# Kernel optimization log

Measured on AMD Instinct MI355X. Metric: run time of the kernel, lower is better.

## Reference

```python
import jax, jax.numpy as jnp
import numpy as np

N, E, F_IN, F_EXP, H, C = 8192, 65536, 3247, 7993, 3, 512
HC = H * C
NEG_SLOPE = 0.2


def setup_inputs() -> dict:
    key = jax.random.key(0)
    ks = jax.random.split(key, 40)
    s = 0.02
    rnd = lambda k, *sh: (jax.random.normal(k, sh, jnp.float32) * s)
    d = {}
    d['x'] = jax.random.normal(ks[0], (N, F_IN), jnp.float32)
    d['edge_index'] = jax.random.randint(ks[1], (2, E), 0, N, jnp.int32)
    d['exp'] = jax.random.normal(ks[2], (N, F_EXP), jnp.float32)
    # GATv2 layer 1 (in=3247)
    d['w1l'] = rnd(ks[3], F_IN, HC); d['b1l'] = rnd(ks[4], HC)
    d['w1r'] = rnd(ks[5], F_IN, HC); d['b1r'] = rnd(ks[6], HC)
    d['a1'] = rnd(ks[7], H, C);      d['o1'] = rnd(ks[8], HC)
    # GATv2 layer 2 (in=1536)
    d['w2l'] = rnd(ks[9], HC, HC);  d['b2l'] = rnd(ks[10], HC)
    d['w2r'] = rnd(ks[11], HC, HC); d['b2r'] = rnd(ks[12], HC)
    d['a2'] = rnd(ks[13], H, C);     d['o2'] = rnd(ks[14], HC)
    # GATv2 layer 3 (in=1536)
    d['w3l'] = rnd(ks[15], HC, HC); d['b3l'] = rnd(ks[16], HC)
    d['w3r'] = rnd(ks[17], HC, HC); d['b3r'] = rnd(ks[18], HC)
    d['a3'] = rnd(ks[19], H, C);     d['o3'] = rnd(ks[20], HC)
    # encoder: 7993 -> 4000 -> 1500 -> 512
    d['e1w'] = rnd(ks[21], F_EXP, 4000); d['e1b'] = rnd(ks[22], 4000)
    d['e2w'] = rnd(ks[23], 4000, 1500);  d['e2b'] = rnd(ks[24], 1500)
    d['e3w'] = rnd(ks[25], 1500, 512);   d['e3b'] = rnd(ks[26], 512)
    # head: 2048 -> 1024 -> 512 -> 1
    d['l1w'] = rnd(ks[27], HC + 512, 1024); d['l1b'] = rnd(ks[28], 1024)
    d['l2w'] = rnd(ks[29], 1024, 512);      d['l2b'] = rnd(ks[30], 512)
    d['l3w'] = rnd(ks[31], 512, 1);         d['l3b'] = rnd(ks[32], 1)
    return d


def gatv2(h, src, dst, wl, bl, wr, br, att, out_bias):
    # PyG GATv2Conv: e_ij = a^T LeakyReLU(W_l h_j + W_r h_i), softmax over j per target i,
    # out_i = sum_j alpha_ij * (W_l h_j), concat heads, + bias.
    xl = (h @ wl + bl).reshape(N, H, C)
    xr = (h @ wr + br).reshape(N, H, C)
    e = jax.nn.leaky_relu(xl[src] + xr[dst], NEG_SLOPE)      # [E', H, C]
    logit = jnp.einsum('ehc,hc->eh', e, att)                  # [E', H]
    m = jax.ops.segment_max(logit, dst, num_segments=N)       # [N, H]
    p = jnp.exp(logit - m[dst])
    z = jax.ops.segment_sum(p, dst, num_segments=N)
    alpha = p / z[dst]                                        # segment softmax
    out = jax.ops.segment_sum(alpha[:, :, None] * xl[src], dst, num_segments=N)
    return out.reshape(N, HC) + out_bias


def reference(x, edge_index, exp,
              w1l, b1l, w1r, b1r, a1, o1,
              w2l, b2l, w2r, b2r, a2, o2,
              w3l, b3l, w3r, b3r, a3, o3,
              e1w, e1b, e2w, e2b, e3w, e3b,
              l1w, l1b, l2w, l2b, l3w, l3b):
    loops = jnp.arange(N, dtype=edge_index.dtype)
    src = jnp.concatenate([edge_index[0], loops])  # add_self_loops=True (PyG default)
    dst = jnp.concatenate([edge_index[1], loops])
    h = jax.nn.relu(gatv2(x, src, dst, w1l, b1l, w1r, b1r, a1, o1))
    h = jax.nn.relu(gatv2(h, src, dst, w2l, b2l, w2r, b2r, a2, o2))
    h = jax.nn.relu(gatv2(h, src, dst, w3l, b3l, w3r, b3r, a3, o3))
    cell = jax.nn.relu(exp @ e1w + e1b)
    cell = jax.nn.relu(cell @ e2w + e2b)
    cell = cell @ e3w + e3b
    z = jnp.concatenate([h, cell], axis=1)  # [N, 2048]
    z = jax.nn.relu(z @ l1w + l1b)
    z = jax.nn.relu(z @ l2w + l2b)
    return z @ l3w + l3b  # [N, 1]
```

## Files before the change

kernel.cpp:

```cpp
#include <hip/hip_runtime.h>
#include <stdint.h>

#define NN 8192
#define NE 65536
#define ET (NE + NN)
#define F_IN   3247
#define F_IN_P 3264
#define F_EXP   7993
#define F_EXP_P 8000

typedef __attribute__((ext_vector_type(8))) short bf16x8;
typedef __attribute__((ext_vector_type(4))) float f32x4;

typedef const __attribute__((address_space(1))) void gvoid_t;
typedef __attribute__((address_space(3))) void lvoid_t;

__device__ __forceinline__ float bf2f(uint16_t u) {
  union { uint32_t i; float f; } v; v.i = ((uint32_t)u) << 16; return v.f;
}
__device__ __forceinline__ uint16_t f2bf(float f) {
  union { float f; uint32_t i; } v; v.f = f;
  uint32_t r = v.i + 0x7fffu + ((v.i >> 16) & 1u);
  return (uint16_t)(r >> 16);
}

__device__ __forceinline__ void gld_lds16(const void* g, void* l) {
  __builtin_amdgcn_global_load_lds((gvoid_t*)g, (lvoid_t*)l, 16, 0, 0);
}

#define SBAR() __builtin_amdgcn_sched_barrier(0)
#define BARRIER() do { SBAR(); __builtin_amdgcn_s_barrier(); SBAR(); } while (0)
#define VMCNT(n) asm volatile("s_waitcnt vmcnt(" #n ")" ::: "memory")
#define MFMA16(a, b, c) __builtin_amdgcn_mfma_f32_16x16x32_bf16(a, b, c, 0, 0, 0)

__device__ __forceinline__ void stage4(const char* src, char* dst, size_t Kb) {
#pragma unroll
  for (int j = 0; j < 4; ++j)
    gld_lds16(src + (size_t)(j * 64) * Kb, dst + j * 8192);
}

#define KTILE(T, BUF)                                                          \
  do {                                                                         \
    const char* aB_  = smem + (BUF) + arow;                                    \
    const char* bB_  = smem + 65536 + (BUF) + brow_o;                          \
    const char* aBn_ = smem + ((BUF) ^ 32768) + arow;                          \
    const bool nls = ((T) + 2 < nk);                                           \
    const bool nlr = ((T) + 1 < nk);                                           \
                        \
    if (nlr) { VMCNT(8); } else { VMCNT(0); }                                  \
    _Pragma("unroll")                                                          \
    for (int n = 0; n < 2; ++n) {                                              \
      b01[n * 2]     = *(const bf16x8*)(bB_ + n * 2048 + sw0);                 \
      b01[n * 2 + 1] = *(const bf16x8*)(bB_ + n * 2048 + sw1);                 \
    }                                                                          \
    _Pragma("unroll")                                                          \
    for (int n = 0; n < 2; ++n) {                                              \
      b23[n * 2]     = *(const bf16x8*)(bB_ + (n + 2) * 2048 + sw0);           \
      b23[n * 2 + 1] = *(const bf16x8*)(bB_ + (n + 2) * 2048 + sw1);           \
    }                                                                          \
    SBAR();                                                                    \
    __builtin_amdgcn_s_setprio(1);                                             \
    _Pragma("unroll")                                                          \
    for (int m = 0; m < 4; ++m)                                                \
      _Pragma("unroll")                                                        \
      for (int n = 0; n < 2; ++n) {                                            \
        acc[m][n] = MFMA16(a03[m * 2],     b01[n * 2],     acc[m][n]);         \
        acc[m][n] = MFMA16(a03[m * 2 + 1], b01[n * 2 + 1], acc[m][n]);         \
      }                                                                        \
    __builtin_amdgcn_s_setprio(0);                                             \
    BARRIER();                                                                 \
                                        \
    _Pragma("unroll")                                                          \
    for (int m = 0; m < 4; ++m) {                                              \
      a47[m * 2]     = *(const bf16x8*)(aB_ + (m + 4) * 2048 + sw0);           \
      a47[m * 2 + 1] = *(const bf16x8*)(aB_ + (m + 4) * 2048 + sw1);           \
    }                                                                          \
    SBAR();                                                                    \
    __builtin_amdgcn_s_setprio(1);                                             \
    _Pragma("unroll")                                                          \
    for (int m = 0; m < 4; ++m)                                                \
      _Pragma("unroll")                                                        \
      for (int n = 0; n < 2; ++n) {                                            \
        acc[m][n + 2] = MFMA16(a03[m * 2],     b23[n * 2],     acc[m][n + 2]); \
        acc[m][n + 2] = MFMA16(a03[m * 2 + 1], b23[n * 2 + 1], acc[m][n + 2]); \
      }                                                                        \
    __builtin_amdgcn_s_setprio(0);                                             \
    BARRIER();                                                                 \
                       \
    if (nls) stage4(pA + (size_t)((T) + 2) * 128, sA + (BUF), Kb);             \
    _Pragma("unroll")                                                          \
    for (int n = 0; n < 2; ++n) {                                              \
      b01[n * 2]     = *(const bf16x8*)(bB_ + n * 2048 + sw0);                 \
      b01[n * 2 + 1] = *(const bf16x8*)(bB_ + n * 2048 + sw1);                 \
    }                                                                          \
    SBAR();                                                                    \
    __builtin_amdgcn_s_setprio(1);                                             \
    _Pragma("unroll")                                                          \
    for (int m = 0; m < 4; ++m)                                                \
      _Pragma("unroll")                                                        \
      for (int n = 0; n < 2; ++n) {                                            \
        acc[m + 4][n + 2] = MFMA16(a47[m * 2],     b23[n * 2],     acc[m + 4][n + 2]); \
        acc[m + 4][n + 2] = MFMA16(a47[m * 2 + 1], b23[n * 2 + 1], acc[m + 4][n + 2]); \
      }                                                                        \
    __builtin_amdgcn_s_setprio(0);                                             \
    BARRIER();                                                                 \
       \
    if (nls)      { VMCNT(8); }                                                \
    else if (nlr) { VMCNT(4); }                                                \
    if (nlr) {                                                                 \
      _Pragma("unroll")                                                        \
      for (int m = 0; m < 4; ++m) {                                            \
        a03[m * 2]     = *(const bf16x8*)(aBn_ + m * 2048 + sw0);              \
        a03[m * 2 + 1] = *(const bf16x8*)(aBn_ + m * 2048 + sw1);              \
      }                                                                        \
    }                                                                          \
    if (nls) stage4(pB + (size_t)((T) + 2) * 128, sB + (BUF), Kb);             \
    SBAR();                                                                    \
    __builtin_amdgcn_s_setprio(1);                                             \
    _Pragma("unroll")                                                          \
    for (int m = 0; m < 4; ++m)                                                \
      _Pragma("unroll")                                                        \
      for (int n = 0; n < 2; ++n) {                                            \
        acc[m + 4][n] = MFMA16(a47[m * 2],     b01[n * 2],     acc[m + 4][n]); \
        acc[m + 4][n] = MFMA16(a47[m * 2 + 1], b01[n * 2 + 1], acc[m + 4][n]); \
      }                                                                        \
    __builtin_amdgcn_s_setprio(0);                                             \
    BARRIER();                                                                 \
  } while (0)

__global__ __launch_bounds__(512, 2)
void gemm256(const uint16_t* __restrict__ A, const uint16_t* __restrict__ Bt,
             const float* __restrict__ bias, int biasN, int relu,
             uint16_t* __restrict__ C, int Kp, int ldc, int nbn)
{
  extern __shared__ char smem[];
  const int tid = threadIdx.x;
  const int w = tid >> 6, lane = tid & 63;
  const int wr = w >> 2, wc = w & 3;
  const int fr = lane & 15, g = lane >> 4;

  const int nwg = (int)gridDim.x;
  const int id = (int)blockIdx.x;
  const int q = nwg >> 3, r = nwg & 7;
  const int xcd = id & 7, idx = id >> 3;
  const int wg = (xcd < r ? xcd * (q + 1) : r * (q + 1) + (xcd - r) * q) + idx;
  const int brow = (wg / nbn) * 256, bcol = (wg % nbn) * 256;

  const size_t Kb = (size_t)Kp * 2;

  const int srow = tid >> 3;
  const int sswz = ((tid & 7) ^ (srow & 7)) * 16;
  const char* pA = (const char*)A + (size_t)(brow + srow) * Kb + sswz;
  const char* pB = (const char*)Bt + (size_t)(bcol + srow) * Kb + sswz;
  char* sA = smem + w * 1024;
  char* sB = smem + 65536 + w * 1024;

  const int sw0 = (g ^ (fr & 7)) * 16;
  const int sw1 = ((g + 4) ^ (fr & 7)) * 16;
  const int arow = (wr * 128 + fr) * 128;
  const int brow_o = (wc * 64 + fr) * 128;

  f32x4 acc[8][4];
#pragma unroll
  for (int m = 0; m < 8; ++m)
#pragma unroll
    for (int n = 0; n < 4; ++n) acc[m][n] = (f32x4){0.f, 0.f, 0.f, 0.f};
  bf16x8 a03[8], a47[8], b01[4], b23[4];

  stage4(pA, sA, Kb);
  stage4(pB, sB, Kb);
  stage4(pA + 128, sA + 32768, Kb);
  stage4(pB + 128, sB + 32768, Kb);
  VMCNT(8);
  BARRIER();
  {
    const char* aB = smem + arow;
#pragma unroll
    for (int m = 0; m < 4; ++m) {
      a03[m * 2]     = *(const bf16x8*)(aB + m * 2048 + sw0);
      a03[m * 2 + 1] = *(const bf16x8*)(aB + m * 2048 + sw1);
    }
  }
  SBAR();

  const int nk = Kp >> 6;
  for (int t = 0; t < nk; t += 2) {
    KTILE(t, 0);
    if (t + 1 < nk) KTILE(t + 1, 32768);
  }

#pragma unroll
  for (int m = 0; m < 8; ++m) {
    const int row = brow + wr * 128 + m * 16 + g * 4;
#pragma unroll
    for (int n = 0; n < 4; ++n) {
      const int col = bcol + wc * 64 + n * 16 + fr;
      const float bv = (col < biasN) ? bias[col] : 0.f;
#pragma unroll
      for (int j = 0; j < 4; ++j) {
        float v = acc[m][n][j] + bv;
        if (relu) v = fmaxf(v, 0.f);
        C[(size_t)(row + j) * ldc + col] = f2bf(v);
      }
    }
  }
}

__global__ __launch_bounds__(256)
void gemm_bt(const uint16_t* __restrict__ A, const uint16_t* __restrict__ Bt,
             const float* __restrict__ bias, int biasN, int relu,
             uint16_t* __restrict__ C, int Kp, int ldc)
{
  __shared__ uint16_t As[128 * 32];
  __shared__ uint16_t Bs[128 * 32];
  const int tid  = threadIdx.x;
  const int wave = tid >> 6, lane = tid & 63;
  const int brow = blockIdx.x * 128, bcol = blockIdx.y * 128;
  const int wr = wave >> 1, wc = wave & 1;
  const int fr = lane & 15, g = lane >> 4;

  f32x4 acc[4][4];
#pragma unroll
  for (int m = 0; m < 4; ++m)
#pragma unroll
    for (int n = 0; n < 4; ++n) acc[m][n] = (f32x4){0.f, 0.f, 0.f, 0.f};

  const int rA = tid >> 2;
  const int kc = (tid & 3) * 8;
  const uint16_t* aptr = A  + (size_t)(brow + rA) * Kp + kc;
  const uint16_t* bptr = Bt + (size_t)(bcol + rA) * Kp + kc;
  char* ldsA = (char*)As + wave * 1024;
  char* ldsB = (char*)Bs + wave * 1024;
  const size_t rowskip = (size_t)64 * Kp;

  const int nk = Kp >> 5;
  for (int kt = 0; kt < nk; ++kt) {
    __syncthreads();
    gld_lds16(aptr,           ldsA);
    gld_lds16(aptr + rowskip, ldsA + 4096);
    gld_lds16(bptr,           ldsB);
    gld_lds16(bptr + rowskip, ldsB + 4096);
    aptr += 32; bptr += 32;
    __syncthreads();

    bf16x8 af[4], bfr[4];
#pragma unroll
    for (int m = 0; m < 4; ++m)
      af[m] = *(const bf16x8*)&As[(wr * 64 + m * 16 + fr) * 32 + g * 8];
#pragma unroll
    for (int n = 0; n < 4; ++n)
      bfr[n] = *(const bf16x8*)&Bs[(wc * 64 + n * 16 + fr) * 32 + g * 8];
#pragma unroll
    for (int m = 0; m < 4; ++m)
#pragma unroll
      for (int n = 0; n < 4; ++n)
        acc[m][n] = MFMA16(af[m], bfr[n], acc[m][n]);
  }

#pragma unroll
  for (int m = 0; m < 4; ++m) {
    const int row = brow + wr * 64 + m * 16 + g * 4;
#pragma unroll
    for (int n = 0; n < 4; ++n) {
      const int col = bcol + wc * 64 + n * 16 + fr;
      const float bv = (col < biasN) ? bias[col] : 0.f;
#pragma unroll
      for (int j = 0; j < 4; ++j) {
        float v = acc[m][n][j] + bv;
        if (relu) v = fmaxf(v, 0.f);
        C[(size_t)(row + j) * ldc + col] = f2bf(v);
      }
    }
  }
}

__global__ __launch_bounds__(256)
void cvt_pad(const float* __restrict__ in, uint16_t* __restrict__ out, int cols, int colsPad)
{
  const int r = blockIdx.y;
  const int c = (blockIdx.x * 256 + threadIdx.x) * 2;
  if (c >= colsPad) return;
  const float* ip = in + (size_t)r * cols;
  const float v0 = (c < cols)     ? ip[c]     : 0.f;
  const float v1 = (c + 1 < cols) ? ip[c + 1] : 0.f;
  const uint32_t pk = (uint32_t)f2bf(v0) | ((uint32_t)f2bf(v1) << 16);
  *(uint32_t*)(out + (size_t)r * colsPad + c) = pk;
}

__global__ __launch_bounds__(256)
void transpose_w(const float* __restrict__ W, uint16_t* __restrict__ Wt,
                 int K, int N, int Kp, int Np)
{
  __shared__ float t[32][33];
  const int tx = threadIdx.x, ty = threadIdx.y;
  const int k0 = blockIdx.x * 32, n0 = blockIdx.y * 32;
#pragma unroll
  for (int j = 0; j < 4; ++j) {
    const int k = k0 + ty + j * 8, n = n0 + tx;
    t[ty + j * 8][tx] = (k < K && n < N) ? W[(size_t)k * N + n] : 0.f;
  }
  __syncthreads();
#pragma unroll
  for (int j = 0; j < 4; ++j) {
    const int n = n0 + ty + j * 8, k = k0 + tx;
    Wt[(size_t)n * Kp + k] = f2bf(t[tx][ty + j * 8]);
  }
}

__global__ void concat_bias(const float* __restrict__ bl, const float* __restrict__ br,
                            float* __restrict__ out)
{
  const int i = blockIdx.x * 256 + threadIdx.x;
  if (i < 1536) out[i] = bl[i];
  else if (i < 3072) out[i] = br[i - 1536];
}

__global__ void count_deg(const int* __restrict__ ei, int* __restrict__ counts)
{
  const int e = blockIdx.x * 256 + threadIdx.x;
  if (e >= ET) return;
  const int d = (e < NE) ? ei[NE + e] : (e - NE);
  atomicAdd(&counts[d], 1);
}

__global__ __launch_bounds__(1024)
void scan_deg(const int* __restrict__ counts, int* __restrict__ row_start, int* __restrict__ cursor)
{
  __shared__ int part[1024];
  const int tid = threadIdx.x;
  int loc[8], pre[8], s = 0;
#pragma unroll
  for (int j = 0; j < 8; ++j) { loc[j] = counts[tid * 8 + j]; pre[j] = s; s += loc[j]; }
  part[tid] = s;
  __syncthreads();
  for (int o = 1; o < 1024; o <<= 1) {
    const int v = part[tid];
    const int a = (tid >= o) ? part[tid - o] : 0;
    __syncthreads();
    part[tid] = v + a;
    __syncthreads();
  }
  const int excl = part[tid] - s;
#pragma unroll
  for (int j = 0; j < 8; ++j) {
    const int v = excl + pre[j];
    row_start[tid * 8 + j] = v;
    cursor[tid * 8 + j]    = v;
  }
  if (tid == 1023) row_start[8192] = excl + s;
}

__global__ void scatter_e(const int* __restrict__ ei, int* __restrict__ cursor,
                          int* __restrict__ csr_src, int* __restrict__ csr_dst)
{
  const int e = blockIdx.x * 256 + threadIdx.x;
  if (e >= ET) return;
  const int sx = (e < NE) ? ei[e]      : (e - NE);
  const int d  = (e < NE) ? ei[NE + e] : (e - NE);
  const int pos = atomicAdd(&cursor[d], 1);
  csr_src[pos] = sx;
  csr_dst[pos] = d;
}

__global__ __launch_bounds__(256)
void gat_logits_n(const uint16_t* __restrict__ xlr, int ld,
                  const int* __restrict__ csr_src, const int* __restrict__ row_start,
                  const float* __restrict__ att, float* __restrict__ logit)
{
  const int node = (blockIdx.x << 2) + (threadIdx.x >> 6);
  const int lane = threadIdx.x & 63;

  float av[3][8];
#pragma unroll
  for (int h = 0; h < 3; ++h) {
    const float4 a0 = *(const float4*)(att + h * 512 + lane * 8);
    const float4 a1 = *(const float4*)(att + h * 512 + lane * 8 + 4);
    av[h][0] = a0.x; av[h][1] = a0.y; av[h][2] = a0.z; av[h][3] = a0.w;
    av[h][4] = a1.x; av[h][5] = a1.y; av[h][6] = a1.z; av[h][7] = a1.w;
  }

  const bf16x8* pr = (const bf16x8*)(xlr + (size_t)node * ld + 1536);
  float xr[3][8];
#pragma unroll
  for (int h = 0; h < 3; ++h) {
    const bf16x8 v = pr[h * 64 + lane];
#pragma unroll
    for (int j = 0; j < 8; ++j) xr[h][j] = bf2f((uint16_t)v[j]);
  }

  const int s0 = row_start[node], s1 = row_start[node + 1];
  for (int s = s0; s < s1; ++s) {
    const bf16x8* pl = (const bf16x8*)(xlr + (size_t)csr_src[s] * ld);
    float hacc[3];
#pragma unroll
    for (int h = 0; h < 3; ++h) {
      const bf16x8 vl = pl[h * 64 + lane];
      float sacc = 0.f;
#pragma unroll
      for (int j = 0; j < 8; ++j) {
        float v = bf2f((uint16_t)vl[j]) + xr[h][j];
        v = v > 0.f ? v : 0.2f * v;
        sacc += v * av[h][j];
      }
      hacc[h] = sacc;
    }
#pragma unroll
    for (int o = 32; o; o >>= 1) {
      hacc[0] += __shfl_xor(hacc[0], o);
      hacc[1] += __shfl_xor(hacc[1], o);
      hacc[2] += __shfl_xor(hacc[2], o);
    }
    if (lane == 0) {
      float* op = logit + (size_t)s * 3;
      op[0] = hacc[0]; op[1] = hacc[1]; op[2] = hacc[2];
    }
  }
}

__global__ __launch_bounds__(256)
void gat_aggregate(const float* __restrict__ logit, const int* __restrict__ csr_src,
                   const int* __restrict__ row_start, const uint16_t* __restrict__ xl, int ldx,
                   const float* __restrict__ ob, uint16_t* __restrict__ out, int ldc)
{
  const int i = blockIdx.x;
  const int tid = threadIdx.x;
  const int s0 = row_start[i], s1 = row_start[i + 1];

  float m0 = -1e30f, m1 = -1e30f, m2 = -1e30f, z0 = 0.f, z1 = 0.f, z2 = 0.f;
  for (int s = s0; s < s1; ++s) {
    const float* lp = logit + (size_t)s * 3;
    float l0 = lp[0], l1 = lp[1], l2 = lp[2];
    float n0 = fmaxf(m0, l0); z0 = z0 * __expf(m0 - n0) + __expf(l0 - n0); m0 = n0;
    float n1 = fmaxf(m1, l1); z1 = z1 * __expf(m1 - n1) + __expf(l1 - n1); m1 = n1;
    float n2 = fmaxf(m2, l2); z2 = z2 * __expf(m2 - n2) + __expf(l2 - n2); m2 = n2;
  }
  const float r0 = 1.f / z0, r1 = 1.f / z1, r2 = 1.f / z2;

  float accl[3], acch[3];
#pragma unroll
  for (int h = 0; h < 3; ++h) { accl[h] = 0.f; acch[h] = 0.f; }
  for (int s = s0; s < s1; ++s) {
    const float* lp = logit + (size_t)s * 3;
    float wv[3];
    wv[0] = __expf(lp[0] - m0) * r0;
    wv[1] = __expf(lp[1] - m1) * r1;
    wv[2] = __expf(lp[2] - m2) * r2;
    const uint32_t* px = (const uint32_t*)(xl + (size_t)csr_src[s] * ldx);
#pragma unroll
    for (int h = 0; h < 3; ++h) {
      const uint32_t u = px[h * 256 + tid];
      accl[h] += wv[h] * bf2f((uint16_t)u);
      acch[h] += wv[h] * bf2f((uint16_t)(u >> 16));
    }
  }
#pragma unroll
  for (int h = 0; h < 3; ++h) {
    const int c = h * 512 + 2 * tid;
    float v0 = fmaxf(accl[h] + ob[c], 0.f);
    float v1 = fmaxf(acch[h] + ob[c + 1], 0.f);
    const uint32_t pk = (uint32_t)f2bf(v0) | ((uint32_t)f2bf(v1) << 16);
    *(uint32_t*)(out + (size_t)i * ldc + c) = pk;
  }
}

__global__ __launch_bounds__(256)
void final_dot(const uint16_t* __restrict__ z2, const float* __restrict__ w,
               const float* __restrict__ b, float* __restrict__ out)
{
  const int row  = blockIdx.x * 4 + (threadIdx.x >> 6);
  const int lane = threadIdx.x & 63;
  const uint16_t* p = z2 + (size_t)row * 512;
  float s = 0.f;
#pragma unroll
  for (int j = 0; j < 8; ++j) { const int c = lane + j * 64; s += bf2f(p[c]) * w[c]; }
#pragma unroll
  for (int o = 32; o; o >>= 1) s += __shfl_xor(s, o);
  if (lane == 0) out[row] = s + b[0];
}

extern "C" void kernel_launch(void* const* d_in, const int* in_sizes, int n_in,
                              void* d_out, int out_size, void* d_ws, size_t ws_size,
                              hipStream_t stream)
{
  (void)in_sizes; (void)n_in; (void)out_size; (void)ws_size;

  const float* x    = (const float*)d_in[0];
  const int*   ei   = (const int*)  d_in[1];
  const float* expm = (const float*)d_in[2];
  const float* w1l = (const float*)d_in[3];  const float* b1l = (const float*)d_in[4];
  const float* w1r = (const float*)d_in[5];  const float* b1r = (const float*)d_in[6];
  const float* a1  = (const float*)d_in[7];  const float* o1  = (const float*)d_in[8];
  const float* w2l = (const float*)d_in[9];  const float* b2l = (const float*)d_in[10];
  const float* w2r = (const float*)d_in[11]; const float* b2r = (const float*)d_in[12];
  const float* a2  = (const float*)d_in[13]; const float* o2  = (const float*)d_in[14];
  const float* w3l = (const float*)d_in[15]; const float* b3l = (const float*)d_in[16];
  const float* w3r = (const float*)d_in[17]; const float* b3r = (const float*)d_in[18];
  const float* a3  = (const float*)d_in[19]; const float* o3  = (const float*)d_in[20];
  const float* e1w = (const float*)d_in[21]; const float* e1b = (const float*)d_in[22];
  const float* e2w = (const float*)d_in[23]; const float* e2b = (const float*)d_in[24];
  const float* e3w = (const float*)d_in[25]; const float* e3b = (const float*)d_in[26];
  const float* l1w = (const float*)d_in[27]; const float* l1b = (const float*)d_in[28];
  const float* l2w = (const float*)d_in[29]; const float* l2b = (const float*)d_in[30];
  const float* l3w = (const float*)d_in[31]; const float* l3b = (const float*)d_in[32];
  float* out = (float*)d_out;

  hipFuncSetAttribute((const void*)gemm256, hipFuncAttributeMaxDynamicSharedMemorySize, 131072);

  char* ws = (char*)d_ws;
  size_t off = 0;
  auto take = [&](size_t b) { char* p = ws + off; off += (b + 255) & ~(size_t)255; return p; };

  int*      counts    = (int*)take((size_t)NN * 4);
  int*      row_start = (int*)take((size_t)(NN + 1) * 4);
  int*      cursor    = (int*)take((size_t)NN * 4);
  int*      csr_src   = (int*)take((size_t)ET * 4);
  int*      csr_dst   = (int*)take((size_t)ET * 4);
  float*    logits    = (float*)take((size_t)ET * 3 * 4);
  float*    bc1       = (float*)take(3072 * 4);
  float*    bc2       = (float*)take(3072 * 4);
  float*    bc3       = (float*)take(3072 * 4);
  uint16_t* zbuf      = (uint16_t*)take((size_t)NN * 2048 * 2);
  char*     regA      = take((size_t)NN * F_EXP_P * 2);
  char*     regW      = take((size_t)4096 * F_EXP_P * 2);
  char*     regC      = take((size_t)NN * 4096 * 2 + (size_t)NN * 1536 * 2);

  uint16_t* xbf   = (uint16_t*)regA;
  uint16_t* expbf = (uint16_t*)regA;
  uint16_t* wT    = (uint16_t*)regW;
  uint16_t* xlr   = (uint16_t*)regC;
  uint16_t* hbuf  = (uint16_t*)(regC + (size_t)NN * 3072 * 2);
  uint16_t* cell1 = (uint16_t*)regC;
  uint16_t* cell2 = (uint16_t*)(regC + (size_t)NN * 4096 * 2);
  uint16_t* zz1   = (uint16_t*)regC;
  uint16_t* zz2   = (uint16_t*)(regC + (size_t)NN * 1024 * 2);

  hipMemsetAsync(counts, 0, (size_t)NN * 4, stream);
  count_deg<<<(ET + 255) / 256, 256, 0, stream>>>(ei, counts);
  scan_deg<<<1, 1024, 0, stream>>>(counts, row_start, cursor);
  scatter_e<<<(ET + 255) / 256, 256, 0, stream>>>(ei, cursor, csr_src, csr_dst);
  concat_bias<<<12, 256, 0, stream>>>(b1l, b1r, bc1);
  concat_bias<<<12, 256, 0, stream>>>(b2l, b2r, bc2);
  concat_bias<<<12, 256, 0, stream>>>(b3l, b3r, bc3);

  cvt_pad<<<dim3((F_IN_P / 2 + 255) / 256, NN), 256, 0, stream>>>(x, xbf, F_IN, F_IN_P);
  transpose_w<<<dim3(F_IN_P / 32, 1536 / 32), dim3(32, 8), 0, stream>>>(w1l, wT, F_IN, 1536, F_IN_P, 1536);
  transpose_w<<<dim3(F_IN_P / 32, 1536 / 32), dim3(32, 8), 0, stream>>>(w1r, wT + (size_t)1536 * F_IN_P, F_IN, 1536, F_IN_P, 1536);
  gemm256<<<32 * 12, 512, 131072, stream>>>(xbf, wT, bc1, 3072, 0, xlr, F_IN_P, 3072, 12);
  gat_logits_n<<<NN / 4, 256, 0, stream>>>(xlr, 3072, csr_src, row_start, a1, logits);
  gat_aggregate<<<NN, 256, 0, stream>>>(logits, csr_src, row_start, xlr, 3072, o1, hbuf, 1536);

  transpose_w<<<dim3(48, 48), dim3(32, 8), 0, stream>>>(w2l, wT, 1536, 1536, 1536, 1536);
  transpose_w<<<dim3(48, 48), dim3(32, 8), 0, stream>>>(w2r, wT + (size_t)1536 * 1536, 1536, 1536, 1536, 1536);
  gemm256<<<32 * 12, 512, 131072, stream>>>(hbuf, wT, bc2, 3072, 0, xlr, 1536, 3072, 12);
  gat_logits_n<<<NN / 4, 256, 0, stream>>>(xlr, 3072, csr_src, row_start, a2, logits);
  gat_aggregate<<<NN, 256, 0, stream>>>(logits, csr_src, row_start, xlr, 3072, o2, hbuf, 1536);

  transpose_w<<<dim3(48, 48), dim3(32, 8), 0, stream>>>(w3l, wT, 1536, 1536, 1536, 1536);
  transpose_w<<<dim3(48, 48), dim3(32, 8), 0, stream>>>(w3r, wT + (size_t)1536 * 1536, 1536, 1536, 1536, 1536);
  gemm256<<<32 * 12, 512, 131072, stream>>>(hbuf, wT, bc3, 3072, 0, xlr, 1536, 3072, 12);
  gat_logits_n<<<NN / 4, 256, 0, stream>>>(xlr, 3072, csr_src, row_start, a3, logits);
  gat_aggregate<<<NN, 256, 0, stream>>>(logits, csr_src, row_start, xlr, 3072, o3, zbuf, 2048);

  cvt_pad<<<dim3((F_EXP_P / 2 + 255) / 256, NN), 256, 0, stream>>>(expm, expbf, F_EXP, F_EXP_P);
  transpose_w<<<dim3(F_EXP_P / 32, 4096 / 32), dim3(32, 8), 0, stream>>>(e1w, wT, F_EXP, 4000, F_EXP_P, 4096);
  gemm256<<<32 * 16, 512, 131072, stream>>>(expbf, wT, e1b, 4000, 1, cell1, F_EXP_P, 4096, 16);
  transpose_w<<<dim3(4096 / 32, 1536 / 32), dim3(32, 8), 0, stream>>>(e2w, wT, 4000, 1500, 4096, 1536);
  gemm256<<<32 * 6, 512, 131072, stream>>>(cell1, wT, e2b, 1500, 1, cell2, 4096, 1536, 6);
  transpose_w<<<dim3(1536 / 32, 512 / 32), dim3(32, 8), 0, stream>>>(e3w, wT, 1500, 512, 1536, 512);
  gemm_bt<<<dim3(64, 4), 256, 0, stream>>>(cell2, wT, e3b, 512, 0, zbuf + 1536, 1536, 2048);

  transpose_w<<<dim3(2048 / 32, 1024 / 32), dim3(32, 8), 0, stream>>>(l1w, wT, 2048, 1024, 2048, 1024);
  gemm256<<<32 * 4, 512, 131072, stream>>>(zbuf, wT, l1b, 1024, 1, zz1, 2048, 1024, 4);
  transpose_w<<<dim3(1024 / 32, 512 / 32), dim3(32, 8), 0, stream>>>(l2w, wT, 1024, 512, 1024, 512);
  gemm_bt<<<dim3(64, 4), 256, 0, stream>>>(zz1, wT, l2b, 512, 1, zz2, 1024, 512);
  final_dot<<<NN / 4, 256, 0, stream>>>(zz2, l3w, l3b, out);
}
```

Baseline: 1.547 ms.

## Fuse GAT logits and softmax-aggregate into one online-softmax kernel

Merges the per-edge logit kernel and the aggregate kernel into a single wave-per-node kernel. It computes each edge's logit and folds it straight into an online softmax with accumulation over the same loaded source features. This removes the logits buffer round trip, a second gather of xl rows, and one launch per layer. Separately, it switches the head's first linear layer from gemm256 to the gemm_bt kernel with a different grid, which may suit the small 1024-column output better or worse.

```diff
diff --git a/kernel.cpp b/kernel.cpp
--- a/kernel.cpp
+++ b/kernel.cpp
@@ -363,42 +363,49 @@
 }
 
 __global__ __launch_bounds__(256)
-void gat_logits_n(const uint16_t* __restrict__ xlr, int ld,
-                  const int* __restrict__ csr_src, const int* __restrict__ row_start,
-                  const float* __restrict__ att, float* __restrict__ logit)
+void gat_fused(const uint16_t* __restrict__ xlr, int ld,
+               const int* __restrict__ csr_src, const int* __restrict__ row_start,
+               const float* __restrict__ att, const float* __restrict__ ob,
+               uint16_t* __restrict__ out, int ldc)
 {
   const int node = (blockIdx.x << 2) + (threadIdx.x >> 6);
   const int lane = threadIdx.x & 63;
 
-  float av[3][8];
+  float av[3][8], xr[3][8];
+  const bf16x8* pr = (const bf16x8*)(xlr + (size_t)node * ld + 1536);
 #pragma unroll
   for (int h = 0; h < 3; ++h) {
     const float4 a0 = *(const float4*)(att + h * 512 + lane * 8);
     const float4 a1 = *(const float4*)(att + h * 512 + lane * 8 + 4);
     av[h][0] = a0.x; av[h][1] = a0.y; av[h][2] = a0.z; av[h][3] = a0.w;
     av[h][4] = a1.x; av[h][5] = a1.y; av[h][6] = a1.z; av[h][7] = a1.w;
-  }
-
-  const bf16x8* pr = (const bf16x8*)(xlr + (size_t)node * ld + 1536);
-  float xr[3][8];
-#pragma unroll
-  for (int h = 0; h < 3; ++h) {
     const bf16x8 v = pr[h * 64 + lane];
 #pragma unroll
     for (int j = 0; j < 8; ++j) xr[h][j] = bf2f((uint16_t)v[j]);
   }
+
+  float m[3] = {-1e30f, -1e30f, -1e30f};
+  float z[3] = {0.f, 0.f, 0.f};
+  float acc[3][8];
+#pragma unroll
+  for (int h = 0; h < 3; ++h)
+#pragma unroll
+    for (int j = 0; j < 8; ++j) acc[h][j] = 0.f;
 
   const int s0 = row_start[node], s1 = row_start[node + 1];
   for (int s = s0; s < s1; ++s) {
     const bf16x8* pl = (const bf16x8*)(xlr + (size_t)csr_src[s] * ld);
+    bf16x8 vl[3];
+#pragma unroll
+    for (int h = 0; h < 3; ++h) vl[h] = pl[h * 64 + lane];
+
     float hacc[3];
 #pragma unroll
     for (int h = 0; h < 3; ++h) {
-      const bf16x8 vl = pl[h * 64 + lane];
       float sacc = 0.f;
 #pragma unroll
       for (int j = 0; j < 8; ++j) {
-        float v = bf2f((uint16_t)vl[j]) + xr[h][j];
+        float v = bf2f((uint16_t)vl[h][j]) + xr[h][j];
         v = v > 0.f ? v : 0.2f * v;
         sacc += v * av[h][j];
       }
@@ -410,56 +417,32 @@
       hacc[1] += __shfl_xor(hacc[1], o);
       hacc[2] += __shfl_xor(hacc[2], o);
     }
-    if (lane == 0) {
-      float* op = logit + (size_t)s * 3;
-      op[0] = hacc[0]; op[1] = hacc[1]; op[2] = hacc[2];
-    }
-  }
-}
-
-__global__ __launch_bounds__(256)
-void gat_aggregate(const float* __restrict__ logit, const int* __restrict__ csr_src,
-                   const int* __restrict__ row_start, const uint16_t* __restrict__ xl, int ldx,
-                   const float* __restrict__ ob, uint16_t* __restrict__ out, int ldc)
-{
-  const int i = blockIdx.x;
-  const int tid = threadIdx.x;
-  const int s0 = row_start[i], s1 = row_start[i + 1];
-
-  float m0 = -1e30f, m1 = -1e30f, m2 = -1e30f, z0 = 0.f, z1 = 0.f, z2 = 0.f;
-  for (int s = s0; s < s1; ++s) {
-    const float* lp = logit + (size_t)s * 3;
-    float l0 = lp[0], l1 = lp[1], l2 = lp[2];
-    float n0 = fmaxf(m0, l0); z0 = z0 * __expf(m0 - n0) + __expf(l0 - n0); m0 = n0;
-    float n1 = fmaxf(m1, l1); z1 = z1 * __expf(m1 - n1) + __expf(l1 - n1); m1 = n1;
-    float n2 = fmaxf(m2, l2); z2 = z2 * __expf(m2 - n2) + __expf(l2 - n2); m2 = n2;
-  }
-  const float r0 = 1.f / z0, r1 = 1.f / z1, r2 = 1.f / z2;
-
-  float accl[3], acch[3];
-#pragma unroll
-  for (int h = 0; h < 3; ++h) { accl[h] = 0.f; acch[h] = 0.f; }
-  for (int s = s0; s < s1; ++s) {
-    const float* lp = logit + (size_t)s * 3;
-    float wv[3];
-    wv[0] = __expf(lp[0] - m0) * r0;
-    wv[1] = __expf(lp[1] - m1) * r1;
-    wv[2] = __expf(lp[2] - m2) * r2;
-    const uint32_t* px = (const uint32_t*)(xl + (size_t)csr_src[s] * ldx);
 #pragma unroll
     for (int h = 0; h < 3; ++h) {
-      const uint32_t u = px[h * 256 + tid];
-      accl[h] += wv[h] * bf2f((uint16_t)u);
-      acch[h] += wv[h] * bf2f((uint16_t)(u >> 16));
-    }
-  }
+      const float nm = fmaxf(m[h], hacc[h]);
+      const float sc = __expf(m[h] - nm);
+      const float p  = __expf(hacc[h] - nm);
+      z[h] = z[h] * sc + p;
+#pragma unroll
+      for (int j = 0; j < 8; ++j)
+        acc[h][j] = acc[h][j] * sc + p * bf2f((uint16_t)vl[h][j]);
+      m[h] = nm;
+    }
+  }
+
 #pragma unroll
   for (int h = 0; h < 3; ++h) {
-    const int c = h * 512 + 2 * tid;
-    float v0 = fmaxf(accl[h] + ob[c], 0.f);
-    float v1 = fmaxf(acch[h] + ob[c + 1], 0.f);
-    const uint32_t pk = (uint32_t)f2bf(v0) | ((uint32_t)f2bf(v1) << 16);
-    *(uint32_t*)(out + (size_t)i * ldc + c) = pk;
+    const float rz = 1.f / z[h];
+    const float4 b0 = *(const float4*)(ob + h * 512 + lane * 8);
+    const float4 b1 = *(const float4*)(ob + h * 512 + lane * 8 + 4);
+    float bv[8] = {b0.x, b0.y, b0.z, b0.w, b1.x, b1.y, b1.z, b1.w};
+    bf16x8 pk;
+#pragma unroll
+    for (int j = 0; j < 8; ++j) {
+      const float v = fmaxf(acc[h][j] * rz + bv[j], 0.f);
+      pk[j] = (short)f2bf(v);
+    }
+    *(bf16x8*)(out + (size_t)node * ldc + h * 512 + lane * 8) = pk;
   }
 }
 
@@ -515,7 +498,6 @@
   int*      cursor    = (int*)take((size_t)NN * 4);
   int*      csr_src   = (int*)take((size_t)ET * 4);
   int*      csr_dst   = (int*)take((size_t)ET * 4);
-  float*    logits    = (float*)take((size_t)ET * 3 * 4);
   float*    bc1       = (float*)take(3072 * 4);
   float*    bc2       = (float*)take(3072 * 4);
   float*    bc3       = (float*)take(3072 * 4);
@@ -546,20 +528,17 @@
   transpose_w<<<dim3(F_IN_P / 32, 1536 / 32), dim3(32, 8), 0, stream>>>(w1l, wT, F_IN, 1536, F_IN_P, 1536);
   transpose_w<<<dim3(F_IN_P / 32, 1536 / 32), dim3(32, 8), 0, stream>>>(w1r, wT + (size_t)1536 * F_IN_P, F_IN, 1536, F_IN_P, 1536);
   gemm256<<<32 * 12, 512, 131072, stream>>>(xbf, wT, bc1, 3072, 0, xlr, F_IN_P, 3072, 12);
-  gat_logits_n<<<NN / 4, 256, 0, stream>>>(xlr, 3072, csr_src, row_start, a1, logits);
-  gat_aggregate<<<NN, 256, 0, stream>>>(logits, csr_src, row_start, xlr, 3072, o1, hbuf, 1536);
+  gat_fused<<<NN / 4, 256, 0, stream>>>(xlr, 3072, csr_src, row_start, a1, o1, hbuf, 1536);
 
   transpose_w<<<dim3(48, 48), dim3(32, 8), 0, stream>>>(w2l, wT, 1536, 1536, 1536, 1536);
   transpose_w<<<dim3(48, 48), dim3(32, 8), 0, stream>>>(w2r, wT + (size_t)1536 * 1536, 1536, 1536, 1536, 1536);
   gemm256<<<32 * 12, 512, 131072, stream>>>(hbuf, wT, bc2, 3072, 0, xlr, 1536, 3072, 12);
-  gat_logits_n<<<NN / 4, 256, 0, stream>>>(xlr, 3072, csr_src, row_start, a2, logits);
-  gat_aggregate<<<NN, 256, 0, stream>>>(logits, csr_src, row_start, xlr, 3072, o2, hbuf, 1536);
+  gat_fused<<<NN / 4, 256, 0, stream>>>(xlr, 3072, csr_src, row_start, a2, o2, hbuf, 1536);
 
   transpose_w<<<dim3(48, 48), dim3(32, 8), 0, stream>>>(w3l, wT, 1536, 1536, 1536, 1536);
   transpose_w<<<dim3(48, 48), dim3(32, 8), 0, stream>>>(w3r, wT + (size_t)1536 * 1536, 1536, 1536, 1536, 1536);
   gemm256<<<32 * 12, 512, 131072, stream>>>(hbuf, wT, bc3, 3072, 0, xlr, 1536, 3072, 12);
-  gat_logits_n<<<NN / 4, 256, 0, stream>>>(xlr, 3072, csr_src, row_start, a3, logits);
-  gat_aggregate<<<NN, 256, 0, stream>>>(logits, csr_src, row_start, xlr, 3072, o3, zbuf, 2048);
+  gat_fused<<<NN / 4, 256, 0, stream>>>(xlr, 3072, csr_src, row_start, a3, o3, zbuf, 2048);
 
   cvt_pad<<<dim3((F_EXP_P / 2 + 255) / 256, NN), 256, 0, stream>>>(expm, expbf, F_EXP, F_EXP_P);
   transpose_w<<<dim3(F_EXP_P / 32, 4096 / 32), dim3(32, 8), 0, stream>>>(e1w, wT, F_EXP, 4000, F_EXP_P, 4096);
@@ -570,7 +549,7 @@
   gemm_bt<<<dim3(64, 4), 256, 0, stream>>>(cell2, wT, e3b, 512, 0, zbuf + 1536, 1536, 2048);
 
   transpose_w<<<dim3(2048 / 32, 1024 / 32), dim3(32, 8), 0, stream>>>(l1w, wT, 2048, 1024, 2048, 1024);
-  gemm256<<<32 * 4, 512, 131072, stream>>>(zbuf, wT, l1b, 1024, 1, zz1, 2048, 1024, 4);
+  gemm_bt<<<dim3(64, 8), 256, 0, stream>>>(zbuf, wT, l1b, 1024, 1, zz1, 2048, 1024);
   transpose_w<<<dim3(1024 / 32, 512 / 32), dim3(32, 8), 0, stream>>>(l2w, wT, 1024, 512, 1024, 512);
   gemm_bt<<<dim3(64, 4), 256, 0, stream>>>(zz1, wT, l2b, 512, 1, zz2, 1024, 512);
   final_dot<<<NN / 4, 256, 0, stream>>>(zz2, l3w, l3b, out);
```

Result: faster. 1.468 ms (-5.1%).
